# Kernel tuning notes

Hardware: AMD Instinct MI355X
Metric: run time of the kernel (lower is better)

## Reference

```python
import jax, jax.numpy as jnp
import numpy as np

INPUT_DIM = 4096
OUTPUT_DIM = 4096
N_MAG_BITS = 3  # inference_sequence = [0, 3]: magnitude bits 0..2, sign bit at index 3
N_TOKENS = 8192
DESIRED_STD = np.sqrt(2.0 / INPUT_DIM)  # kaiming fan_in std target


def _ste(hard, soft):
    # straight-through estimator: forward = hard, backward = identity on soft
    return soft + jax.lax.stop_gradient(hard - soft)


def to_bit(x):
    # latent float -> {0,1} bit plane
    return _ste((x >= 0).astype(x.dtype), x)


def to_sign(x):
    # latent float -> {-1,+1} sign plane
    return _ste(jnp.where(x >= 0, 1.0, -1.0).astype(x.dtype), x)


def setup_inputs() -> dict:
    key = jax.random.key(0)
    k1, k2, k3 = jax.random.split(key, 3)
    x = jax.random.normal(k1, (N_TOKENS, INPUT_DIM), dtype=jnp.float32)
    mag = jax.random.normal(k2, (N_MAG_BITS, INPUT_DIM, OUTPUT_DIM), dtype=jnp.float32)
    sign_bit = jax.random.normal(k3, (INPUT_DIM, OUTPUT_DIM), dtype=jnp.float32)
    return {"x": x, "mag": mag, "sign_bit": sign_bit}


def reference(x, mag, sign_bit):
    # calculate_number: reconstruct weight from bit planes
    # w = sign * sum_i bit_i * 2^{-(i+1)}
    bits = to_bit(mag)  # [K, in, out]
    place = (2.0 ** -(jnp.arange(1, N_MAG_BITS + 1, dtype=jnp.float32)))  # [K]
    magnitude = jnp.einsum("kio,k->io", bits, place)
    w = to_sign(sign_bit) * magnitude  # [in, out]
    # calc_scaling_factor on detached weight (cpu/numpy round-trip in original -> constant)
    alpha = DESIRED_STD / (jnp.std(jax.lax.stop_gradient(w)) + 1e-12)
    w = w * alpha
    # F.linear(x, W.T) == x @ W
    return jnp.matmul(x, w)
```

## Files before the change

kernel.cpp:

```cpp
#include <hip/hip_runtime.h>
#include <hip/hip_bf16.h>
#include <cstdint>
#include <cstddef>

#define IN_DIM 4096
#define OUT_DIM 4096
#define NTOK 8192
#define PLANE (IN_DIM * OUT_DIM)
#define NPACK_BLOCKS 4096

#define BM 256
#define BN 256
#define BK 64
#define KTILES (IN_DIM / BK)

typedef int i32x4_t __attribute__((ext_vector_type(4)));

__device__ inline void async_load16(void* lds, const void* g) {
    __builtin_amdgcn_global_load_lds(
        (const __attribute__((address_space(1))) char*)g,
        (__attribute__((address_space(3))) char*)lds,
        16, 0, 0);
}

__global__ __launch_bounds__(256) void pack_kernel(const float* __restrict__ mag,
                                                   const float* __restrict__ sgn,
                                                   signed char* __restrict__ wT,
                                                   int* __restrict__ partials) {
    __shared__ short tile[64 * 68];
    __shared__ int red2[4], reds[4];
    const int t = threadIdx.x;
    const int o0 = blockIdx.x * 64, i0 = blockIdx.y * 64;
    const int oq = t & 15, ir = t >> 4;
    int lk2 = 0, lsk = 0;
    #pragma unroll
    for (int r = 0; r < 4; ++r) {
        const int ilo = r * 16 + ir;
        const size_t idx = (size_t)(i0 + ilo) * OUT_DIM + o0 + oq * 4;
        const float4 m0 = *(const float4*)(mag + idx);
        const float4 m1 = *(const float4*)(mag + idx + (size_t)PLANE);
        const float4 m2 = *(const float4*)(mag + idx + 2 * (size_t)PLANE);
        const float4 sv = *(const float4*)(sgn + idx);
        short4 c;
        {
            int k = ((m0.x >= 0.f) ? 4 : 0) | ((m1.x >= 0.f) ? 2 : 0) | ((m2.x >= 0.f) ? 1 : 0);
            int cd = (sv.x >= 0.f) ? k : -k; lk2 += k * k; lsk += cd; c.x = (short)cd;
        }
        {
            int k = ((m0.y >= 0.f) ? 4 : 0) | ((m1.y >= 0.f) ? 2 : 0) | ((m2.y >= 0.f) ? 1 : 0);
            int cd = (sv.y >= 0.f) ? k : -k; lk2 += k * k; lsk += cd; c.y = (short)cd;
        }
        {
            int k = ((m0.z >= 0.f) ? 4 : 0) | ((m1.z >= 0.f) ? 2 : 0) | ((m2.z >= 0.f) ? 1 : 0);
            int cd = (sv.z >= 0.f) ? k : -k; lk2 += k * k; lsk += cd; c.z = (short)cd;
        }
        {
            int k = ((m0.w >= 0.f) ? 4 : 0) | ((m1.w >= 0.f) ? 2 : 0) | ((m2.w >= 0.f) ? 1 : 0);
            int cd = (sv.w >= 0.f) ? k : -k; lk2 += k * k; lsk += cd; c.w = (short)cd;
        }
        *(short4*)&tile[ilo * 68 + oq * 4] = c;
    }
    #pragma unroll
    for (int off = 32; off > 0; off >>= 1) {
        lk2 += __shfl_down(lk2, off);
        lsk += __shfl_down(lsk, off);
    }
    const int wv = t >> 6, ln = t & 63;
    if (ln == 0) { red2[wv] = lk2; reds[wv] = lsk; }
    __syncthreads();
    if (t == 0) {
        const int bid = blockIdx.y * gridDim.x + blockIdx.x;
        partials[bid] = red2[0] + red2[1] + red2[2] + red2[3];
        partials[NPACK_BLOCKS + bid] = reds[0] + reds[1] + reds[2] + reds[3];
    }
    const int iq = t & 15, orr = t >> 4;
    #pragma unroll
    for (int r = 0; r < 4; ++r) {
        const int olo = r * 16 + orr;
        char4 w4;
        w4.x = (signed char)tile[(iq * 4 + 0) * 68 + olo];
        w4.y = (signed char)tile[(iq * 4 + 1) * 68 + olo];
        w4.z = (signed char)tile[(iq * 4 + 2) * 68 + olo];
        w4.w = (signed char)tile[(iq * 4 + 3) * 68 + olo];
        *(char4*)&wT[(size_t)(o0 + olo) * IN_DIM + i0 + iq * 4] = w4;
    }
}

__global__ __launch_bounds__(256) void alpha_kernel(const int* __restrict__ partials,
                                                    float* __restrict__ alpha8) {
    __shared__ int red2[4], reds[4];
    const int t = threadIdx.x;
    int k2 = 0, sk = 0;
    for (int i = t; i < NPACK_BLOCKS; i += 256) {
        k2 += partials[i];
        sk += partials[NPACK_BLOCKS + i];
    }
    #pragma unroll
    for (int off = 32; off > 0; off >>= 1) {
        k2 += __shfl_down(k2, off);
        sk += __shfl_down(sk, off);
    }
    const int wv = t >> 6, ln = t & 63;
    if (ln == 0) { red2[wv] = k2; reds[wv] = sk; }
    __syncthreads();
    if (t == 0) {
        const double n = (double)PLANE;
        const double sumk2 = (double)(red2[0] + red2[1] + red2[2] + red2[3]);
        const double sumsk = (double)(reds[0] + reds[1] + reds[2] + reds[3]);
        const double mean = sumsk / (8.0 * n);
        const double e2 = sumk2 / (64.0 * n);
        const double sd = sqrt(e2 - mean * mean);
        *alpha8 = (float)(sqrt(2.0 / (double)IN_DIM) / (sd + 1e-12) * 0.125);
    }
}

__global__ __launch_bounds__(256) void quant_kernel(const float* __restrict__ x,
                                                    signed char* __restrict__ xq,
                                                    float* __restrict__ steps) {
    __shared__ float red[4];
    const int r = blockIdx.x, t = threadIdx.x;
    const float* xr = x + (size_t)r * IN_DIM;
    float4 v[4];
    float am = 0.f;
    #pragma unroll
    for (int p = 0; p < 4; ++p) {
        v[p] = ((const float4*)xr)[p * 256 + t];
        am = fmaxf(am, fmaxf(fmaxf(fabsf(v[p].x), fabsf(v[p].y)),
                             fmaxf(fabsf(v[p].z), fabsf(v[p].w))));
    }
    #pragma unroll
    for (int off = 32; off > 0; off >>= 1) am = fmaxf(am, __shfl_down(am, off));
    const int wv = t >> 6, ln = t & 63;
    if (ln == 0) red[wv] = am;
    __syncthreads();
    am = fmaxf(fmaxf(red[0], red[1]), fmaxf(red[2], red[3]));
    am = fmaxf(am, 1e-30f);
    const float rstep = 127.0f / am;
    if (t == 0) steps[r] = am * (1.0f / 127.0f);
    int* xqi = (int*)(xq + (size_t)r * IN_DIM);
    #pragma unroll
    for (int p = 0; p < 4; ++p) {
        const int q0 = (int)rintf(v[p].x * rstep);
        const int q1 = (int)rintf(v[p].y * rstep);
        const int q2 = (int)rintf(v[p].z * rstep);
        const int q3 = (int)rintf(v[p].w * rstep);
        xqi[p * 256 + t] = (q0 & 0xFF) | ((q1 & 0xFF) << 8) | ((q2 & 0xFF) << 16) | (q3 << 24);
    }
}

__global__ __launch_bounds__(512, 2) void gemm_kernel(const signed char* __restrict__ A,
                                                      const signed char* __restrict__ B,
                                                      float* __restrict__ C,
                                                      const float* __restrict__ alphap,
                                                      const float* __restrict__ steps) {
    __shared__ __align__(16) signed char As[4][BM * BK];
    __shared__ __align__(16) signed char Bs[4][BN * BK];
    const int t = threadIdx.x;
    const int lane = t & 63;
    const int wave = t >> 6;
    const int wm = wave >> 2, wn = wave & 3;
    const int r15 = lane & 15, q = lane >> 4;

    const int raw = blockIdx.x;
    const int wg = (raw & 7) * 64 + (raw >> 3);
    const int m0 = (wg >> 4) * BM;
    const int n0 = (wg & 15) * BN;

    int aoff[8], boff[4];
    #pragma unroll
    for (int i = 0; i < 8; ++i) {
        const int r = wm * 128 + i * 16 + r15;
        aoff[i] = r * BK + ((q ^ ((r >> 1) & 3)) << 4);
    }
    #pragma unroll
    for (int i = 0; i < 4; ++i) {
        const int r = wn * 64 + i * 16 + r15;
        boff[i] = r * BK + ((q ^ ((r >> 1) & 3)) << 4);
    }

    const int c0 = t, c1 = t + 512;
    const int ra0 = c0 >> 2, ra1 = c1 >> 2;
    const int sc0 = (((c0 & 3) ^ ((c0 >> 3) & 3)) << 4);
    const int sc1 = (((c1 & 3) ^ ((c1 >> 3) & 3)) << 4);
    const size_t srcA0 = (size_t)(m0 + ra0) * IN_DIM + sc0;
    const size_t srcA1 = (size_t)(m0 + ra1) * IN_DIM + sc1;
    const size_t srcB0 = (size_t)(n0 + ra0) * IN_DIM + sc0;
    const size_t srcB1 = (size_t)(n0 + ra1) * IN_DIM + sc1;

    i32x4_t acc[8][4] = {};

#define STAGE(kt, buf) do {                                          \
        const int koff_ = (kt) * BK;                                 \
        async_load16(&As[buf][c0 * 16], A + srcA0 + koff_);          \
        async_load16(&As[buf][c1 * 16], A + srcA1 + koff_);          \
        async_load16(&Bs[buf][c0 * 16], B + srcB0 + koff_);          \
        async_load16(&Bs[buf][c1 * 16], B + srcB1 + koff_);          \
    } while (0)

#define COMPUTE(buf) do {                                            \
        i32x4_t a_[8], b_[4];                                        \
        _Pragma("unroll")                                            \
        for (int i = 0; i < 8; ++i)                                  \
            a_[i] = *(const i32x4_t*)&As[buf][aoff[i]];              \
        _Pragma("unroll")                                            \
        for (int i = 0; i < 4; ++i)                                  \
            b_[i] = *(const i32x4_t*)&Bs[buf][boff[i]];              \
        __builtin_amdgcn_s_setprio(1);                               \
        _Pragma("unroll")                                            \
        for (int mt = 0; mt < 8; ++mt)                               \
            _Pragma("unroll")                                        \
            for (int nt = 0; nt < 4; ++nt)                           \
                acc[mt][nt] = __builtin_amdgcn_mfma_i32_16x16x64_i8( \
                    a_[mt], b_[nt], acc[mt][nt], 0, 0, 0);           \
        __builtin_amdgcn_s_setprio(0);                               \
    } while (0)

    STAGE(0, 0); STAGE(1, 1); STAGE(2, 2);

    #pragma unroll 4
    for (int kt = 0; kt < KTILES - 3; ++kt) {
        STAGE(kt + 3, (kt + 3) & 3);
        asm volatile("s_waitcnt vmcnt(12)" ::: "memory");
        __builtin_amdgcn_s_barrier();
        COMPUTE(kt & 3);
        __builtin_amdgcn_s_barrier();
    }
    asm volatile("s_waitcnt vmcnt(8)" ::: "memory");
    __builtin_amdgcn_s_barrier();
    COMPUTE((KTILES - 3) & 3);
    asm volatile("s_waitcnt vmcnt(4)" ::: "memory");
    __builtin_amdgcn_s_barrier();
    COMPUTE((KTILES - 2) & 3);
    asm volatile("s_waitcnt vmcnt(0)" ::: "memory");
    __builtin_amdgcn_s_barrier();
    COMPUTE((KTILES - 1) & 3);

#undef STAGE
#undef COMPUTE

    const float alpha8 = *alphap;
    #pragma unroll
    for (int mt = 0; mt < 8; ++mt) {
        const int mbase = m0 + wm * 128 + mt * 16 + q * 4;
        const float s0 = alpha8 * steps[mbase + 0];
        const float s1 = alpha8 * steps[mbase + 1];
        const float s2 = alpha8 * steps[mbase + 2];
        const float s3 = alpha8 * steps[mbase + 3];
        #pragma unroll
        for (int nt = 0; nt < 4; ++nt) {
            const int n = n0 + wn * 64 + nt * 16 + r15;
            float* cp = C + (size_t)mbase * OUT_DIM + n;
            cp[0 * OUT_DIM] = (float)acc[mt][nt][0] * s0;
            cp[1 * OUT_DIM] = (float)acc[mt][nt][1] * s1;
            cp[2 * OUT_DIM] = (float)acc[mt][nt][2] * s2;
            cp[3 * OUT_DIM] = (float)acc[mt][nt][3] * s3;
        }
    }
}

extern "C" void kernel_launch(void* const* d_in, const int* in_sizes, int n_in,
                              void* d_out, int out_size, void* d_ws, size_t ws_size,
                              hipStream_t stream) {
    const float* x   = (const float*)d_in[0];
    const float* mag = (const float*)d_in[1];
    const float* sgn = (const float*)d_in[2];
    float* out = (float*)d_out;

    char* ws = (char*)d_ws;
    int* partials = (int*)ws;
    float* alphap = (float*)(ws + 32768);
    float* steps  = (float*)(ws + 65536);
    signed char* wT = (signed char*)(ws + 131072);
    signed char* xq = (signed char*)(ws + 131072 + (size_t)PLANE);

    pack_kernel<<<dim3(OUT_DIM / 64, IN_DIM / 64), 256, 0, stream>>>(mag, sgn, wT, partials);
    quant_kernel<<<NTOK, 256, 0, stream>>>(x, xq, steps);
    alpha_kernel<<<1, 256, 0, stream>>>(partials, alphap);
    gemm_kernel<<<dim3((NTOK / BM) * (OUT_DIM / BN)), 512, 0, stream>>>(xq, wT, out, alphap, steps);
}
```

Measured before the change: 553.1 us.

## Split int8 MFMA tile compute into four barrier-synchronised phases

Each K-tile's compute is split into four phases. Each phase loads two A fragments from LDS (the B fragments are loaded once, in the first phase) and then issues eight MFMAs. Barriers are placed before and after each phase so the waves in a workgroup stay in lockstep, interleaving LDS reads and MFMA bursts across waves. This also lowers peak register pressure from the A fragments. The cost is many more barriers per tile, eight instead of one, which can add stalls.

```diff
diff --git a/kernel.cpp b/kernel.cpp
--- a/kernel.cpp
+++ b/kernel.cpp
@@ -188,6 +188,7 @@
     const size_t srcB1 = (size_t)(n0 + ra1) * IN_DIM + sc1;
 
     i32x4_t acc[8][4] = {};
+    i32x4_t b_[4];
 
 #define STAGE(kt, buf) do {                                          \
         const int koff_ = (kt) * BK;                                 \
@@ -197,22 +198,31 @@
         async_load16(&Bs[buf][c1 * 16], B + srcB1 + koff_);          \
     } while (0)
 
-#define COMPUTE(buf) do {                                            \
-        i32x4_t a_[8], b_[4];                                        \
-        _Pragma("unroll")                                            \
-        for (int i = 0; i < 8; ++i)                                  \
-            a_[i] = *(const i32x4_t*)&As[buf][aoff[i]];              \
-        _Pragma("unroll")                                            \
-        for (int i = 0; i < 4; ++i)                                  \
-            b_[i] = *(const i32x4_t*)&Bs[buf][boff[i]];              \
+#define PHASE(buf, p) do {                                           \
+        const i32x4_t a0_ = *(const i32x4_t*)&As[buf][aoff[2*(p)]];  \
+        const i32x4_t a1_ = *(const i32x4_t*)&As[buf][aoff[2*(p)+1]];\
+        if ((p) == 0) {                                              \
+            b_[0] = *(const i32x4_t*)&Bs[buf][boff[0]];              \
+            b_[1] = *(const i32x4_t*)&Bs[buf][boff[1]];              \
+            b_[2] = *(const i32x4_t*)&Bs[buf][boff[2]];              \
+            b_[3] = *(const i32x4_t*)&Bs[buf][boff[3]];              \
+        }                                                            \
+        __builtin_amdgcn_s_barrier();                                \
         __builtin_amdgcn_s_setprio(1);                               \
         _Pragma("unroll")                                            \
-        for (int mt = 0; mt < 8; ++mt)                               \
-            _Pragma("unroll")                                        \
-            for (int nt = 0; nt < 4; ++nt)                           \
-                acc[mt][nt] = __builtin_amdgcn_mfma_i32_16x16x64_i8( \
-                    a_[mt], b_[nt], acc[mt][nt], 0, 0, 0);           \
+        for (int nt = 0; nt < 4; ++nt)                               \
+            acc[2*(p)][nt] = __builtin_amdgcn_mfma_i32_16x16x64_i8(  \
+                a0_, b_[nt], acc[2*(p)][nt], 0, 0, 0);               \
+        _Pragma("unroll")                                            \
+        for (int nt = 0; nt < 4; ++nt)                               \
+            acc[2*(p)+1][nt] = __builtin_amdgcn_mfma_i32_16x16x64_i8(\
+                a1_, b_[nt], acc[2*(p)+1][nt], 0, 0, 0);             \
         __builtin_amdgcn_s_setprio(0);                               \
+        __builtin_amdgcn_s_barrier();                                \
+    } while (0)
+
+#define COMPUTE4(buf) do {                                           \
+        PHASE(buf, 0); PHASE(buf, 1); PHASE(buf, 2); PHASE(buf, 3);  \
     } while (0)
 
     STAGE(0, 0); STAGE(1, 1); STAGE(2, 2);
@@ -222,21 +232,21 @@
         STAGE(kt + 3, (kt + 3) & 3);
         asm volatile("s_waitcnt vmcnt(12)" ::: "memory");
         __builtin_amdgcn_s_barrier();
-        COMPUTE(kt & 3);
-        __builtin_amdgcn_s_barrier();
+        COMPUTE4(kt & 3);
     }
     asm volatile("s_waitcnt vmcnt(8)" ::: "memory");
     __builtin_amdgcn_s_barrier();
-    COMPUTE((KTILES - 3) & 3);
+    COMPUTE4((KTILES - 3) & 3);
     asm volatile("s_waitcnt vmcnt(4)" ::: "memory");
     __builtin_amdgcn_s_barrier();
-    COMPUTE((KTILES - 2) & 3);
+    COMPUTE4((KTILES - 2) & 3);
     asm volatile("s_waitcnt vmcnt(0)" ::: "memory");
     __builtin_amdgcn_s_barrier();
-    COMPUTE((KTILES - 1) & 3);
-
+    COMPUTE4((KTILES - 1) & 3);
+
+#undef COMPUTE4
+#undef PHASE
 #undef STAGE
-#undef COMPUTE
 
     const float alpha8 = *alphap;
     #pragma unroll
```

Result: slower. 564.6 us (+2.1%).
